# Optimization experiments

Hardware: AMD Instinct MI355X
Metric: run time of the kernel (lower is better)

Reference implementation:

```python
import jax, jax.numpy as jnp
import numpy as np

N, E = 100000, 1600000
IN_CH, HID, HEADS, OUT_CH = 128, 32, 2, 40
NEG_SLOPE = 0.2
BN_EPS = 1e-5


def _param(key, shape, scale=0.1):
    return scale * jax.random.normal(key, shape, dtype=jnp.float32)


def setup_inputs() -> dict:
    key = jax.random.key(0)
    ks = jax.random.split(key, 24)
    x = jax.random.normal(ks[0], (N, IN_CH), dtype=jnp.float32)
    edge_index = jax.random.randint(ks[1], (2, E), 0, N, dtype=jnp.int32)
    d0 = HEADS * HID  # 64
    inp = {
        'x': x, 'edge_index': edge_index,
        # conv0: in 128 -> 32 per head, concat -> 64
        'W0': _param(ks[2], (IN_CH, HEADS * HID)),
        'as0': _param(ks[3], (HEADS, HID)), 'ad0': _param(ks[4], (HEADS, HID)),
        'b0': jnp.zeros((d0,), jnp.float32),
        'g0': jnp.ones((d0,), jnp.float32), 'bt0': jnp.zeros((d0,), jnp.float32),
        # conv1: 64 -> 32 per head, concat -> 64
        'W1': _param(ks[5], (d0, HEADS * HID)),
        'as1': _param(ks[6], (HEADS, HID)), 'ad1': _param(ks[7], (HEADS, HID)),
        'b1': jnp.zeros((d0,), jnp.float32),
        'g1': jnp.ones((d0,), jnp.float32), 'bt1': jnp.zeros((d0,), jnp.float32),
        # conv2: 64 -> 40 per head, mean over heads -> 40
        'W2': _param(ks[8], (d0, HEADS * OUT_CH)),
        'as2': _param(ks[9], (HEADS, OUT_CH)), 'ad2': _param(ks[10], (HEADS, OUT_CH)),
        'b2': jnp.zeros((OUT_CH,), jnp.float32),
    }
    return inp


def gat_conv(x, src, dst, W, a_src, a_dst, bias, out_ch, concat):
    n = x.shape[0]
    h = (x @ W).reshape(n, HEADS, out_ch)            # [N,H,C]
    alpha_src = jnp.sum(h * a_src, axis=-1)          # [N,H]
    alpha_dst = jnp.sum(h * a_dst, axis=-1)          # [N,H]
    e = jax.nn.leaky_relu(alpha_src[src] + alpha_dst[dst], NEG_SLOPE)  # [E,H]
    # softmax over incoming edges per destination node (self loops guarantee >=1 edge)
    m = jax.ops.segment_max(e, dst, num_segments=n)
    e = jnp.exp(e - m[dst])
    s = jax.ops.segment_sum(e, dst, num_segments=n)
    alpha = e / s[dst]                                # [E,H]
    msg = h[src] * alpha[:, :, None]                  # [E,H,C]
    out = jax.ops.segment_sum(msg, dst, num_segments=n)  # [N,H,C]
    out = out.reshape(n, HEADS * out_ch) if concat else out.mean(axis=1)
    return out + bias


def batch_norm(x, gamma, beta):
    mu = jnp.mean(x, axis=0)
    var = jnp.mean(jnp.square(x - mu), axis=0)
    return gamma * (x - mu) * jax.lax.rsqrt(var + BN_EPS) + beta


def reference(x, edge_index, W0, as0, ad0, b0, g0, bt0,
              W1, as1, ad1, b1, g1, bt1, W2, as2, ad2, b2):
    n = x.shape[0]
    loops = jnp.arange(n, dtype=edge_index.dtype)
    src = jnp.concatenate([edge_index[0], loops])
    dst = jnp.concatenate([edge_index[1], loops])
    h = gat_conv(x, src, dst, W0, as0, ad0, b0, HID, True)
    h = jax.nn.elu(batch_norm(h, g0, bt0))
    h = gat_conv(h, src, dst, W1, as1, ad1, b1, HID, True)
    h = jax.nn.elu(batch_norm(h, g1, bt1))
    return gat_conv(h, src, dst, W2, as2, ad2, b2, OUT_CH, False)
```

## Files before the change

### kernel.cpp

```cpp
#include <hip/hip_runtime.h>
#include <hip/hip_bf16.h>
#include <math.h>


#define NNODES 100000
#define NEDGES 1600000
#define ENTOT  (NEDGES + NNODES)
#define NEG_SLOPE 0.2f
#define BN_EPS 1e-5f

#define NRANGE 8
#define RSIZE  (NNODES/NRANGE)
#define BCAP   262144
#define PBLK   2048
#define NB2    32

typedef unsigned short u16;
typedef unsigned int u32;
typedef unsigned long long u64;
typedef __attribute__((ext_vector_type(8))) short short8;
typedef __attribute__((ext_vector_type(4))) float f32x4;

__device__ __forceinline__ float b2f(u16 u){ union{u32 i; float f;} v; v.i=((u32)u)<<16; return v.f; }
__device__ __forceinline__ float blo(u32 u){ union{u32 i; float f;} v; v.i=u<<16; return v.f; }
__device__ __forceinline__ float bhi(u32 u){ union{u32 i; float f;} v; v.i=u&0xffff0000u; return v.f; }
__device__ __forceinline__ u16 f2b(float x){ __hip_bfloat16 b=__float2bfloat16(x); return *(u16*)&b; }
__device__ __forceinline__ float ldf(const void* p, int i, int f){
  return f ? ((const float*)p)[i] : b2f(((const u16*)p)[i]);
}

__global__ void k_detect(const u16* __restrict__ x, int* __restrict__ flag){
  __shared__ int bad;
  if(threadIdx.x==0) bad=0;
  __syncthreads();
  int cnt=0;
  for(int i=threadIdx.x;i<4096;i+=256){
    u16 v = x[2*i];
    int ex = (v>>7)&0xff;
    if(ex==0xff || (ex==0 && (v&0x7fff)!=0)) cnt++;
  }
  atomicAdd(&bad,cnt);
  __syncthreads();
  if(threadIdx.x==0) flag[0] = (bad>4)?1:0;
}

__global__ __launch_bounds__(256) void k_part2(
    const int* __restrict__ ei, int* __restrict__ gptr, u32* __restrict__ bkt){
  __shared__ int lcnt[NRANGE], gbase[NRANGE];
  int t=threadIdx.x;
  if(t<NRANGE) lcnt[t]=0;
  __syncthreads();
  const int CH=(ENTOT+PBLK-1)/PBLK;
  int beg=blockIdx.x*CH, end=beg+CH; if(end>ENTOT) end=ENTOT;
  int nd[4], ns[4], nr[4], ne=0;
  for(int i=beg+t; i<end; i+=256){
    int d=(i<NEDGES)? ei[NEDGES+i] : (i-NEDGES);
    int s=(i<NEDGES)? ei[i] : d;
    nd[ne]=d; ns[ne]=s; ne++;
  }
  #pragma unroll 4
  for(int k=0;k<ne;k++) nr[k]=atomicAdd(&lcnt[nd[k]/RSIZE],1);
  __syncthreads();
  if(t<NRANGE) gbase[t]=atomicAdd(&gptr[t],lcnt[t]);
  __syncthreads();
  #pragma unroll 4
  for(int k=0;k<ne;k++){
    int r=nd[k]/RSIZE;
    u32 e = ((u32)(nd[k]-r*RSIZE)<<17) | (u32)ns[k];
    __builtin_nontemporal_store(e, &bkt[(size_t)r*BCAP + gbase[r] + nr[k]]);
  }
}

__global__ __launch_bounds__(256) void k_hist4(
    const u32* __restrict__ bkt, const int* __restrict__ gptr, int* __restrict__ lhist){
  __shared__ int lh[RSIZE];
  int t=threadIdx.x;
  for(int i=t;i<RSIZE;i+=256) lh[i]=0;
  __syncthreads();
  int r = blockIdx.x & (NRANGE-1);
  int c = blockIdx.x >> 3;
  int n = gptr[r];
  int per=(n+NB2-1)/NB2;
  int beg=c*per, end=beg+per; if(end>n) end=n;
  const u32* bp = bkt + (size_t)r*BCAP;
  for(int i=beg+t;i<end;i+=256) atomicAdd(&lh[bp[i]>>17],1);
  __syncthreads();
  int* out = lhist + (size_t)(r*NB2+c)*RSIZE;
  for(int i=t;i<RSIZE;i+=256) out[i]=lh[i];
}

__global__ __launch_bounds__(256) void k_sumscan(int* __restrict__ lhist, int* __restrict__ cnt){
  int n = blockIdx.x*256 + threadIdx.x;
  if(n>=NNODES) return;
  int r = n/RSIZE, i = n - r*RSIZE;
  int* base = lhist + (size_t)r*NB2*RSIZE + i;
  int run=0;
  #pragma unroll 8
  for(int c=0;c<NB2;c++){
    int v = base[(size_t)c*RSIZE];
    base[(size_t)c*RSIZE] = run;
    run += v;
  }
  cnt[n]=run;
}

#define SCAN_M (NNODES+1)
#define SCAN_NB ((SCAN_M + 2047)/2048)

__global__ void k_scan_a(const int* __restrict__ cnt, int* __restrict__ bsum){
  __shared__ int red[256];
  int b=blockIdx.x, t=threadIdx.x;
  int base = b*2048 + t*8;
  int s=0;
  #pragma unroll
  for(int j=0;j<8;j++){ int idx=base+j; s += (idx<NNODES)? cnt[idx]:0; }
  red[t]=s; __syncthreads();
  for(int o=128;o>0;o>>=1){ if(t<o) red[t]+=red[t+o]; __syncthreads(); }
  if(t==0) bsum[b]=red[0];
}

__global__ void k_scan_b(int* bsum){
  if(threadIdx.x==0){
    int run=0;
    for(int i=0;i<SCAN_NB;i++){ int v=bsum[i]; bsum[i]=run; run+=v; }
  }
}

__global__ void k_scan_c(const int* __restrict__ cnt, const int* __restrict__ bsum,
                         int* __restrict__ row_ptr){
  __shared__ int lds[256];
  int b=blockIdx.x, t=threadIdx.x;
  int base=b*2048+t*8;
  int v[8]; int s=0;
  #pragma unroll
  for(int j=0;j<8;j++){ int idx=base+j; int x=(idx<NNODES)?cnt[idx]:0; v[j]=s; s+=x; }
  lds[t]=s; __syncthreads();
  for(int o=1;o<256;o<<=1){
    int other=0; if(t>=o) other=lds[t-o];
    __syncthreads();
    lds[t]+=other;
    __syncthreads();
  }
  int texcl = lds[t] - s;
  int off0 = bsum[b] + texcl;
  #pragma unroll
  for(int j=0;j<8;j++){ int idx=base+j; if(idx<SCAN_M) row_ptr[idx]=off0+v[j]; }
}

__global__ __launch_bounds__(256) void k_scatter4(
    const u32* __restrict__ bkt, const int* __restrict__ gptr,
    const int* __restrict__ row_ptr, const int* __restrict__ lhist,
    int* __restrict__ col){
  __shared__ int lofs[RSIZE];
  int t=threadIdx.x;
  int r = blockIdx.x & (NRANGE-1);
  int c = blockIdx.x >> 3;
  int lo = r*RSIZE;
  const int* cb = lhist + (size_t)(r*NB2+c)*RSIZE;
  for(int i=t;i<RSIZE;i+=256) lofs[i] = row_ptr[lo+i] + cb[i];
  __syncthreads();
  int n = gptr[r];
  int per=(n+NB2-1)/NB2;
  int beg=c*per, end=beg+per; if(end>n) end=n;
  const u32* bp = bkt + (size_t)r*BCAP;
  for(int i=beg+t;i<end;i+=256){
    u32 e=bp[i];
    int pos=atomicAdd(&lofs[e>>17],1);
    col[pos]=(int)(e & 0x1FFFF);
  }
}

template<int K, int OUTC, int HID, bool XEXT, bool BN>
__global__ __launch_bounds__(256) void k_gemm_mfma(
    const void* __restrict__ xin, const void* __restrict__ W,
    const void* __restrict__ avs, const void* __restrict__ avd,
    const float2* __restrict__ bnab,
    u16* __restrict__ hout, float* __restrict__ asrc, float* __restrict__ adst,
    const int* __restrict__ flagp)
{
  const int f = flagp[0];
  constexpr int KP = K+8;
  constexpr int RS = OUTC+8;
  constexpr int NT = OUTC/16;
  constexpr int KQ = K/32;
  __shared__ __align__(16) u16 WT[OUTC*KP];
  __shared__ __align__(16) u16 HROW[4*16*RS];
  __shared__ float AVb[2*OUTC];
  __shared__ float2 BB[K];
  int t=threadIdx.x;
  const u16* Wu=(const u16*)W; const float* Wf=(const float*)W;
  for(int i8=t*8; i8<K*OUTC; i8+=256*8){
    int k=i8/OUTC, c0=i8-k*OUTC;
    u16 w8[8];
    if(f){
      const float* wp=Wf+i8;
      float4 a=*(const float4*)wp, b=*(const float4*)(wp+4);
      w8[0]=f2b(a.x);w8[1]=f2b(a.y);w8[2]=f2b(a.z);w8[3]=f2b(a.w);
      w8[4]=f2b(b.x);w8[5]=f2b(b.y);w8[6]=f2b(b.z);w8[7]=f2b(b.w);
    } else {
      uint4 q=*(const uint4*)(Wu+i8);
      w8[0]=q.x&0xffff;w8[1]=q.x>>16;w8[2]=q.y&0xffff;w8[3]=q.y>>16;
      w8[4]=q.z&0xffff;w8[5]=q.z>>16;w8[6]=q.w&0xffff;w8[7]=q.w>>16;
    }
    #pragma unroll
    for(int u=0;u<8;u++) WT[(c0+u)*KP + k] = w8[u];
  }
  for(int idx=t; idx<2*OUTC; idx+=256)
    AVb[idx] = (idx<OUTC)? ldf(avs,idx,f) : ldf(avd,idx-OUTC,f);
  if(BN) for(int idx=t; idx<K; idx+=256) BB[idx]=bnab[idx];
  __syncthreads();

  int wv=t>>6, lane=t&63;
  int m=lane&15, quad=lane>>4;
  int grow0 = blockIdx.x*64 + wv*16;
  int growA = grow0 + m;
  bool avalid = growA < NNODES;
  int growC = avalid ? growA : 0;

  f32x4 acc[NT] = {};
  #pragma unroll
  for(int kq=0;kq<KQ;kq++){
    int k0 = kq*32 + quad*8;
    union{ u32 u[4]; short8 s8; } A;
    if(XEXT && f==1){
      const float* xr=(const float*)xin + (size_t)growC*K + k0;
      float4 p=*(const float4*)xr, q=*(const float4*)(xr+4);
      A.u[0]=f2b(p.x)|((u32)f2b(p.y)<<16);
      A.u[1]=f2b(p.z)|((u32)f2b(p.w)<<16);
      A.u[2]=f2b(q.x)|((u32)f2b(q.y)<<16);
      A.u[3]=f2b(q.z)|((u32)f2b(q.w)<<16);
    } else {
      uint4 q=*(const uint4*)((const u16*)xin + (size_t)growC*K + k0);
      A.u[0]=q.x; A.u[1]=q.y; A.u[2]=q.z; A.u[3]=q.w;
    }
    if(BN){
      #pragma unroll
      for(int j=0;j<4;j++){
        float lo=b2f(A.u[j]&0xffff), hi=b2f(A.u[j]>>16);
        float2 c1=BB[k0+2*j], c2=BB[k0+2*j+1];
        lo=c1.x*lo+c1.y; lo = lo>0.f? lo : __expf(lo)-1.f;
        hi=c2.x*hi+c2.y; hi = hi>0.f? hi : __expf(hi)-1.f;
        A.u[j]=f2b(lo)|((u32)f2b(hi)<<16);
      }
    }
    #pragma unroll
    for(int nt=0;nt<NT;nt++){
      union{ uint4 q; short8 s8; } Bf;
      Bf.q = *(const uint4*)&WT[(nt*16+m)*KP + k0];
      acc[nt] = __builtin_amdgcn_mfma_f32_16x16x32_bf16(A.s8, Bf.s8, acc[nt], 0,0,0);
    }
  }
  u16* hr = &HROW[wv*16*RS];
  #pragma unroll
  for(int nt=0;nt<NT;nt++){
    #pragma unroll
    for(int reg=0;reg<4;reg++)
      hr[(quad*4+reg)*RS + nt*16+m] = f2b(acc[nt][reg]);
  }
  __syncthreads();
  {
    int row=lane&15, task=quad, head=task&1, sd=task>>1;
    float p=0.f;
    const u16* hrow=&hr[row*RS + head*HID];
    const float* av=&AVb[sd*OUTC + head*HID];
    #pragma unroll 8
    for(int c=0;c<HID;c++) p += b2f(hrow[c])*av[c];
    int grow=grow0+row;
    if(grow<NNODES){ (sd? adst:asrc)[grow*2+head]=p; }
  }
  {
    constexpr int CH8 = OUTC/8;
    for(int idx=lane; idx<16*CH8; idx+=64){
      int rr=idx/CH8, c8=idx-rr*CH8;
      int grow=grow0+rr;
      if(grow<NNODES)
        *(uint4*)(hout + (size_t)grow*OUTC + c8*8) = *(const uint4*)&hr[rr*RS + c8*8];
    }
  }
}

template<int OUTC, bool FINAL>
__global__ __launch_bounds__(256) void k_aggf(
  const int* __restrict__ row_ptr, const int* __restrict__ col,
  const u16* __restrict__ hin, const float2* __restrict__ asrc2,
  const float2* __restrict__ adst2, const void* __restrict__ bias,
  u16* __restrict__ houtb, void* __restrict__ outv, const int* __restrict__ flagp)
{
  const int f = flagp[0];
  __shared__ float vbuf[FINAL?32:1][84];
  constexpr int HSPLIT = FINAL ? 5 : 4;
  int t = threadIdx.x;
  int g  = t>>3;
  int cg = t&7;
  int rr = blockIdx.x & 7, jb = blockIdx.x >> 3;
  int lim = RSIZE - jb*32;
  bool ok = g < lim;
  int d = rr*RSIZE + jb*32 + g;
  int base=0, deg=0;
  float2 adv = make_float2(0.f,0.f);
  if(ok){
    base = row_ptr[d];
    deg  = row_ptr[d+1] - base;
    adv  = adst2[d];
  }
  const int* cp = col + base;
  float acc[8]={0,0,0,0,0,0,0,0}, accx0=0.f, accx1=0.f;
  float s0=0.f, s1=0.f;
  for(int j=0;j<deg;j+=2){
    int c0 = cp[j];
    bool v1 = (j+1)<deg;
    int c1 = cp[v1 ? j+1 : j];
    float2 sa = asrc2[c0];
    float2 sb = asrc2[c1];
    const u16* hp0 = hin + (size_t)c0*OUTC;
    const u16* hp1 = hin + (size_t)c1*OUTC;
    uint4 h0 = *(const uint4*)(hp0 + cg*8);
    uint4 h1 = *(const uint4*)(hp1 + cg*8);
    float e0 = sa.x+adv.x; e0 = fmaxf(e0, NEG_SLOPE*e0); e0 = fminf(e0,60.f);
    float e1 = sa.y+adv.y; e1 = fmaxf(e1, NEG_SLOPE*e1); e1 = fminf(e1,60.f);
    float p0 = __expf(e0), p1 = __expf(e1);
    float q0 = sb.x+adv.x; q0 = fmaxf(q0, NEG_SLOPE*q0); q0 = fminf(q0,60.f);
    float q1 = sb.y+adv.y; q1 = fmaxf(q1, NEG_SLOPE*q1); q1 = fminf(q1,60.f);
    float r0 = __expf(q0), r1 = __expf(q1);
    if(!v1){ r0=0.f; r1=0.f; }
    s0 += p0 + r0; s1 += p1 + r1;
    float pa = (cg<HSPLIT)? p0 : p1;
    float pb = (cg<HSPLIT)? r0 : r1;
    acc[0] += pa*blo(h0.x) + pb*blo(h1.x);
    acc[1] += pa*bhi(h0.x) + pb*bhi(h1.x);
    acc[2] += pa*blo(h0.y) + pb*blo(h1.y);
    acc[3] += pa*bhi(h0.y) + pb*bhi(h1.y);
    acc[4] += pa*blo(h0.z) + pb*blo(h1.z);
    acc[5] += pa*bhi(h0.z) + pb*bhi(h1.z);
    acc[6] += pa*blo(h0.w) + pb*blo(h1.w);
    acc[7] += pa*bhi(h0.w) + pb*bhi(h1.w);
    if(FINAL){
      ushort2 ha = *(const ushort2*)(hp0 + 64 + cg*2);
      ushort2 hb = *(const ushort2*)(hp1 + 64 + cg*2);
      accx0 += p1*b2f(ha.x) + r1*b2f(hb.x);
      accx1 += p1*b2f(ha.y) + r1*b2f(hb.y);
    }
  }
  float inv0 = s0>0.f?1.f/s0:0.f, inv1 = s1>0.f?1.f/s1:0.f;
  if(!FINAL){
    if(ok){
      float inv = (cg<4)? inv0 : inv1;
      u16 o8[8];
      #pragma unroll
      for(int k=0;k<8;k++) o8[k]=f2b(acc[k]*inv + ldf(bias,cg*8+k,f));
      uint4 ov;
      ov.x=(u32)o8[0]|((u32)o8[1]<<16); ov.y=(u32)o8[2]|((u32)o8[3]<<16);
      ov.z=(u32)o8[4]|((u32)o8[5]<<16); ov.w=(u32)o8[6]|((u32)o8[7]<<16);
      *(uint4*)(houtb + (size_t)d*64 + cg*8) = ov;
    }
  } else {
    if(ok){
      #pragma unroll
      for(int k=0;k<8;k++)
        vbuf[g][cg*8+k] = acc[k]*((cg<5)?inv0:inv1);
      vbuf[g][64+cg*2]   = accx0*inv1;
      vbuf[g][64+cg*2+1] = accx1*inv1;
    }
    __syncthreads();
    for(int idx=t; idx<32*40; idx+=256){
      int gg=idx/40, ch=idx-gg*40;
      if(gg<lim){
        int dd = rr*RSIZE + jb*32 + gg;
        float res = 0.5f*(vbuf[gg][ch] + vbuf[gg][40+ch]) + ldf(bias,ch,f);
        if(f) ((float*)outv)[(size_t)dd*40+ch] = res;
        else  ((__hip_bfloat16*)outv)[(size_t)dd*40+ch] = __float2bfloat16(res);
      }
    }
  }
}

__global__ __launch_bounds__(256) void k_bnstats(const u16* __restrict__ h, float* __restrict__ stats){
  __shared__ float red[4][128];
  int t=threadIdx.x; int c=t&63; int g=t>>6;
  float s=0.f,q=0.f;
  for(int r=blockIdx.x*4+g; r<NNODES; r+=gridDim.x*4){
    float v=b2f(h[(size_t)r*64+c]); s+=v; q+=v*v;
  }
  red[g][c]=s; red[g][64+c]=q;
  __syncthreads();
  if(t<128){
    float tot=red[0][t]+red[1][t]+red[2][t]+red[3][t];
    atomicAdd(&stats[t], tot);
  }
}

__global__ void k_bnfinal(const float* __restrict__ stats,
                          const void* __restrict__ gm, const void* __restrict__ bt,
                          float2* __restrict__ bnab, const int* __restrict__ flagp){
  const int f = flagp[0];
  int c=threadIdx.x;
  if(c>=64) return;
  float mu=stats[c]*(1.0f/NNODES);
  float var=stats[64+c]*(1.0f/NNODES)-mu*mu;
  var = var>0.f?var:0.f;
  float A = ldf(gm,c,f)*rsqrtf(var+BN_EPS);
  float B = ldf(bt,c,f) - A*mu;
  bnab[c]=make_float2(A,B);
}

extern "C" void kernel_launch(void* const* d_in, const int* in_sizes, int n_in,
                              void* d_out, int out_size, void* d_ws, size_t ws_size,
                              hipStream_t stream){
  const void* x  =d_in[0];
  const int* ei =(const int*)d_in[1];
  const void* W0 =d_in[2];  const void* as0=d_in[3];  const void* ad0=d_in[4];
  const void* b0 =d_in[5];  const void* g0 =d_in[6];  const void* bt0=d_in[7];
  const void* W1 =d_in[8];  const void* as1=d_in[9];  const void* ad1=d_in[10];
  const void* b1 =d_in[11]; const void* g1 =d_in[12]; const void* bt1=d_in[13];
  const void* W2 =d_in[14]; const void* as2=d_in[15]; const void* ad2=d_in[16];
  const void* b2 =d_in[17];

  char* ws=(char*)d_ws;
  size_t off=0;
  auto alloc=[&](size_t bytes)->void*{ void* p=ws+off; off+=(bytes+255)&~(size_t)255; return p; };
  int*    flag   =(int*)   alloc(256);
  int*    row_ptr=(int*)   alloc((size_t)(NNODES+1)*4);
  int*    cnt    =(int*)   alloc((size_t)NNODES*4);
  int*    colx   =(int*)   alloc((size_t)ENTOT*4);
  int*    bsum   =(int*)   alloc((size_t)SCAN_NB*4);
  int*    gptr   =(int*)   alloc(256);
  u32*    bkt    =(u32*)   alloc((size_t)NRANGE*BCAP*4);
  u16*    hA     =(u16*)   alloc((size_t)100032*80*2);
  u16*    hB0    =(u16*)   alloc((size_t)100032*64*2);
  u16*    hB1    =(u16*)   alloc((size_t)100032*64*2);
  float*  asrc   =(float*) alloc((size_t)NNODES*2*4);
  float*  adst   =(float*) alloc((size_t)NNODES*2*4);
  float*  stats  =(float*) alloc(128*4);
  float2* bnab   =(float2*)alloc(64*8);
  int*    lhist  =(int*)hA;

  k_detect<<<1,256,0,stream>>>((const u16*)x, flag);

  (void)hipMemsetAsync(gptr,0,256,stream);
  k_part2  <<<PBLK,256,0,stream>>>(ei,gptr,bkt);
  k_hist4  <<<NRANGE*NB2,256,0,stream>>>(bkt,gptr,lhist);
  k_sumscan<<<(NNODES+255)/256,256,0,stream>>>(lhist,cnt);
  k_scan_a <<<SCAN_NB,256,0,stream>>>(cnt,bsum);
  k_scan_b <<<1,64,0,stream>>>(bsum);
  k_scan_c <<<SCAN_NB,256,0,stream>>>(cnt,bsum,row_ptr);
  k_scatter4<<<NRANGE*NB2,256,0,stream>>>(bkt,gptr,row_ptr,lhist,colx);

  int gG = (NNODES+63)/64;
  int gA = NRANGE * ((RSIZE + 31)/32);
  k_gemm_mfma<128,64,32,true ,false><<<gG,256,0,stream>>>(
      x,W0,as0,ad0,nullptr,hA,asrc,adst,flag);
  k_aggf<64,false><<<gA,256,0,stream>>>(row_ptr,colx,hA,
      (const float2*)asrc,(const float2*)adst,b0,hB0,nullptr,flag);
  (void)hipMemsetAsync(stats,0,512,stream);
  k_bnstats<<<256,256,0,stream>>>(hB0,stats);
  k_bnfinal<<<1,64,0,stream>>>(stats,g0,bt0,bnab,flag);
  k_gemm_mfma<64,64,32,false,true ><<<gG,256,0,stream>>>(
      hB0,W1,as1,ad1,bnab,hA,asrc,adst,flag);
  k_aggf<64,false><<<gA,256,0,stream>>>(row_ptr,colx,hA,
      (const float2*)asrc,(const float2*)adst,b1,hB1,nullptr,flag);
  (void)hipMemsetAsync(stats,0,512,stream);
  k_bnstats<<<256,256,0,stream>>>(hB1,stats);
  k_bnfinal<<<1,64,0,stream>>>(stats,g1,bt1,bnab,flag);
  k_gemm_mfma<64,80,40,false,true ><<<gG,256,0,stream>>>(
      hB1,W2,as2,ad2,bnab,hA,asrc,adst,flag);
  k_aggf<80,true ><<<gA,256,0,stream>>>(row_ptr,colx,hA,
      (const float2*)asrc,(const float2*)adst,b2,nullptr,d_out,flag);

  (void)in_sizes;(void)n_in;(void)out_size;(void)ws_size;
}
```

Measured before the change: 455.2 us.

## Sort each node's neighbors by source range and sync aggregation by sub-band

Adds a per-node pass that reorders each adjacency list into 8 source-node ranges and records the sub-offsets. The aggregation kernels then walk neighbors band by band with a block-wide barrier after each band. This keeps all threads gathering from the same slice of the feature table at once, so L2 can hold it better. The cost is an extra sorting kernel, an extra column array, and barriers that make every thread wait for the slowest node in each band.

```diff
diff --git a/kernel.cpp b/kernel.cpp
--- a/kernel.cpp
+++ b/kernel.cpp
@@ -167,6 +167,37 @@
     u32 e=bp[i];
     int pos=atomicAdd(&lofs[e>>17],1);
     col[pos]=(int)(e & 0x1FFFF);
+  }
+}
+
+__global__ __launch_bounds__(256) void k_binsort(
+    const int* __restrict__ row_ptr, const int* __restrict__ col,
+    int* __restrict__ col2, int* __restrict__ subo){
+  int d = blockIdx.x*256 + threadIdx.x;
+  if(d>=NNODES) return;
+  int b0=row_ptr[d], b1=row_ptr[d+1];
+  u64 cntp=0;
+  for(int j=b0;j<b1;j++){
+    int sb = col[j]/RSIZE;
+    cntp += 1ull << (sb*8);
+  }
+  u64 offp=0; u32 run=0;
+  #pragma unroll
+  for(int sb=0;sb<8;sb++){
+    offp |= (u64)(run&0xffu) << (sb*8);
+    run += (u32)((cntp >> (sb*8)) & 0xff);
+  }
+  int s[8];
+  #pragma unroll
+  for(int sb=0;sb<8;sb++) s[sb] = b0 + (int)((offp>>(sb*8))&0xff);
+  *(int4*)&subo[(size_t)d*8]   = make_int4(s[0],s[1],s[2],s[3]);
+  *(int4*)&subo[(size_t)d*8+4] = make_int4(s[4],s[5],s[6],s[7]);
+  for(int j=b0;j<b1;j++){
+    int c = col[j];
+    int sb = c/RSIZE;
+    int pos = b0 + (int)((offp>>(sb*8))&0xff);
+    offp += 1ull << (sb*8);
+    col2[pos]=c;
   }
 }
 
@@ -281,7 +312,8 @@
 
 template<int OUTC, bool FINAL>
 __global__ __launch_bounds__(256) void k_aggf(
-  const int* __restrict__ row_ptr, const int* __restrict__ col,
+  const int* __restrict__ row_ptr, const int* __restrict__ col2,
+  const int* __restrict__ subo,
   const u16* __restrict__ hin, const float2* __restrict__ asrc2,
   const float2* __restrict__ adst2, const void* __restrict__ bias,
   u16* __restrict__ houtb, void* __restrict__ outv, const int* __restrict__ flagp)
@@ -292,55 +324,65 @@
   int t = threadIdx.x;
   int g  = t>>3;
   int cg = t&7;
+  int lane = t&63;
+  int gb = lane & 56;
   int rr = blockIdx.x & 7, jb = blockIdx.x >> 3;
   int lim = RSIZE - jb*32;
   bool ok = g < lim;
   int d = rr*RSIZE + jb*32 + g;
-  int base=0, deg=0;
+  int dend=0, bs=0;
   float2 adv = make_float2(0.f,0.f);
   if(ok){
-    base = row_ptr[d];
-    deg  = row_ptr[d+1] - base;
+    dend = row_ptr[d+1];
     adv  = adst2[d];
-  }
-  const int* cp = col + base;
+    bs   = subo[(size_t)d*8 + cg];
+  }
+  const u16* hcg = hin + cg*8;
+  const u16* hxg = hin + 64 + cg*2;
   float acc[8]={0,0,0,0,0,0,0,0}, accx0=0.f, accx1=0.f;
   float s0=0.f, s1=0.f;
-  for(int j=0;j<deg;j+=2){
-    int c0 = cp[j];
-    bool v1 = (j+1)<deg;
-    int c1 = cp[v1 ? j+1 : j];
-    float2 sa = asrc2[c0];
-    float2 sb = asrc2[c1];
-    const u16* hp0 = hin + (size_t)c0*OUTC;
-    const u16* hp1 = hin + (size_t)c1*OUTC;
-    uint4 h0 = *(const uint4*)(hp0 + cg*8);
-    uint4 h1 = *(const uint4*)(hp1 + cg*8);
-    float e0 = sa.x+adv.x; e0 = fmaxf(e0, NEG_SLOPE*e0); e0 = fminf(e0,60.f);
-    float e1 = sa.y+adv.y; e1 = fmaxf(e1, NEG_SLOPE*e1); e1 = fminf(e1,60.f);
-    float p0 = __expf(e0), p1 = __expf(e1);
-    float q0 = sb.x+adv.x; q0 = fmaxf(q0, NEG_SLOPE*q0); q0 = fminf(q0,60.f);
-    float q1 = sb.y+adv.y; q1 = fmaxf(q1, NEG_SLOPE*q1); q1 = fminf(q1,60.f);
-    float r0 = __expf(q0), r1 = __expf(q1);
-    if(!v1){ r0=0.f; r1=0.f; }
-    s0 += p0 + r0; s1 += p1 + r1;
-    float pa = (cg<HSPLIT)? p0 : p1;
-    float pb = (cg<HSPLIT)? r0 : r1;
-    acc[0] += pa*blo(h0.x) + pb*blo(h1.x);
-    acc[1] += pa*bhi(h0.x) + pb*bhi(h1.x);
-    acc[2] += pa*blo(h0.y) + pb*blo(h1.y);
-    acc[3] += pa*bhi(h0.y) + pb*bhi(h1.y);
-    acc[4] += pa*blo(h0.z) + pb*blo(h1.z);
-    acc[5] += pa*bhi(h0.z) + pb*bhi(h1.z);
-    acc[6] += pa*blo(h0.w) + pb*blo(h1.w);
-    acc[7] += pa*bhi(h0.w) + pb*bhi(h1.w);
-    if(FINAL){
-      ushort2 ha = *(const ushort2*)(hp0 + 64 + cg*2);
-      ushort2 hb = *(const ushort2*)(hp1 + 64 + cg*2);
-      accx0 += p1*b2f(ha.x) + r1*b2f(hb.x);
-      accx1 += p1*b2f(ha.y) + r1*b2f(hb.y);
-    }
-  }
+
+  for(int sb=0; sb<8; ++sb){
+    int beg = __shfl(bs, gb+sb, 64);
+    int end = (sb<7)? __shfl(bs, gb+sb+1, 64) : dend;
+    for(int j=beg; j<end; j+=2){
+      int c0 = col2[j];
+      bool v1 = (j+1)<end;
+      int c1 = col2[v1 ? j+1 : j];
+      float2 sa = asrc2[c0];
+      float2 sv = asrc2[c1];
+      const u16* hp0 = hcg + (size_t)c0*OUTC;
+      const u16* hp1 = hcg + (size_t)c1*OUTC;
+      uint4 h0 = *(const uint4*)hp0;
+      uint4 h1 = *(const uint4*)hp1;
+      float e0 = sa.x+adv.x; e0 = fmaxf(e0, NEG_SLOPE*e0); e0 = fminf(e0,60.f);
+      float e1 = sa.y+adv.y; e1 = fmaxf(e1, NEG_SLOPE*e1); e1 = fminf(e1,60.f);
+      float p0 = __expf(e0), p1 = __expf(e1);
+      float q0 = sv.x+adv.x; q0 = fmaxf(q0, NEG_SLOPE*q0); q0 = fminf(q0,60.f);
+      float q1 = sv.y+adv.y; q1 = fmaxf(q1, NEG_SLOPE*q1); q1 = fminf(q1,60.f);
+      float r0 = __expf(q0), r1 = __expf(q1);
+      if(!v1){ r0=0.f; r1=0.f; }
+      s0 += p0 + r0; s1 += p1 + r1;
+      float pa = (cg<HSPLIT)? p0 : p1;
+      float pb = (cg<HSPLIT)? r0 : r1;
+      acc[0] += pa*blo(h0.x) + pb*blo(h1.x);
+      acc[1] += pa*bhi(h0.x) + pb*bhi(h1.x);
+      acc[2] += pa*blo(h0.y) + pb*blo(h1.y);
+      acc[3] += pa*bhi(h0.y) + pb*bhi(h1.y);
+      acc[4] += pa*blo(h0.z) + pb*blo(h1.z);
+      acc[5] += pa*bhi(h0.z) + pb*bhi(h1.z);
+      acc[6] += pa*blo(h0.w) + pb*blo(h1.w);
+      acc[7] += pa*bhi(h0.w) + pb*bhi(h1.w);
+      if(FINAL){
+        ushort2 ha = *(const ushort2*)(hxg + (size_t)c0*OUTC);
+        ushort2 hb = *(const ushort2*)(hxg + (size_t)c1*OUTC);
+        accx0 += p1*b2f(ha.x) + r1*b2f(hb.x);
+        accx1 += p1*b2f(ha.y) + r1*b2f(hb.y);
+      }
+    }
+    __syncthreads();
+  }
+
   float inv0 = s0>0.f?1.f/s0:0.f, inv1 = s1>0.f?1.f/s1:0.f;
   if(!FINAL){
     if(ok){
@@ -422,6 +464,8 @@
   int*    row_ptr=(int*)   alloc((size_t)(NNODES+1)*4);
   int*    cnt    =(int*)   alloc((size_t)NNODES*4);
   int*    colx   =(int*)   alloc((size_t)ENTOT*4);
+  int*    colx2  =(int*)   alloc((size_t)ENTOT*4);
+  int*    subo   =(int*)   alloc((size_t)NNODES*8*4);
   int*    bsum   =(int*)   alloc((size_t)SCAN_NB*4);
   int*    gptr   =(int*)   alloc(256);
   u32*    bkt    =(u32*)   alloc((size_t)NRANGE*BCAP*4);
@@ -444,26 +488,27 @@
   k_scan_b <<<1,64,0,stream>>>(bsum);
   k_scan_c <<<SCAN_NB,256,0,stream>>>(cnt,bsum,row_ptr);
   k_scatter4<<<NRANGE*NB2,256,0,stream>>>(bkt,gptr,row_ptr,lhist,colx);
+  k_binsort<<<(NNODES+255)/256,256,0,stream>>>(row_ptr,colx,colx2,subo);
 
   int gG = (NNODES+63)/64;
   int gA = NRANGE * ((RSIZE + 31)/32);
   k_gemm_mfma<128,64,32,true ,false><<<gG,256,0,stream>>>(
       x,W0,as0,ad0,nullptr,hA,asrc,adst,flag);
-  k_aggf<64,false><<<gA,256,0,stream>>>(row_ptr,colx,hA,
+  k_aggf<64,false><<<gA,256,0,stream>>>(row_ptr,colx2,subo,hA,
       (const float2*)asrc,(const float2*)adst,b0,hB0,nullptr,flag);
   (void)hipMemsetAsync(stats,0,512,stream);
   k_bnstats<<<256,256,0,stream>>>(hB0,stats);
   k_bnfinal<<<1,64,0,stream>>>(stats,g0,bt0,bnab,flag);
   k_gemm_mfma<64,64,32,false,true ><<<gG,256,0,stream>>>(
       hB0,W1,as1,ad1,bnab,hA,asrc,adst,flag);
-  k_aggf<64,false><<<gA,256,0,stream>>>(row_ptr,colx,hA,
+  k_aggf<64,false><<<gA,256,0,stream>>>(row_ptr,colx2,subo,hA,
       (const float2*)asrc,(const float2*)adst,b1,hB1,nullptr,flag);
   (void)hipMemsetAsync(stats,0,512,stream);
   k_bnstats<<<256,256,0,stream>>>(hB1,stats);
   k_bnfinal<<<1,64,0,stream>>>(stats,g1,bt1,bnab,flag);
   k_gemm_mfma<64,80,40,false,true ><<<gG,256,0,stream>>>(
       hB1,W2,as2,ad2,bnab,hA,asrc,adst,flag);
-  k_aggf<80,true ><<<gA,256,0,stream>>>(row_ptr,colx,hA,
+  k_aggf<80,true ><<<gA,256,0,stream>>>(row_ptr,colx2,subo,hA,
       (const float2*)asrc,(const float2*)adst,b2,nullptr,d_out,flag);
 
   (void)in_sizes;(void)n_in;(void)out_size;(void)ws_size;
```

New measurement: 525.5 us. 15.5% more time.
